# Kernel tuning notes

Measured on AMD Instinct MI355X. Metric: run time of the kernel, lower is better.

## Reference

```python
import jax, jax.numpy as jnp
import numpy as np

BETA = 0.25


def setup_inputs() -> dict:
    key = jax.random.key(0)
    k1, k2 = jax.random.split(key)
    z = jax.random.normal(k1, (16, 1024, 256), dtype=jnp.float32)
    embedding = jax.random.normal(k2, (8192, 256), dtype=jnp.float32)
    return {"z": z, "embedding": embedding}


def reference(z, embedding):
    e_dim = embedding.shape[-1]
    z_flat = jnp.reshape(z, (-1, e_dim))  # [N, e_dim]
    # d[i,k] = ||z_i||^2 + ||e_k||^2 - 2 z_i . e_k  -> [N, n_e]
    d = (jnp.sum(z_flat ** 2, axis=1, keepdims=True)
         + jnp.sum(embedding ** 2, axis=1)
         - 2.0 * jnp.einsum('nd,kd->nk', z_flat, embedding))
    min_encoding_indices = jnp.argmin(d, axis=1)  # [N]
    z_q = embedding[min_encoding_indices]
    z_q = jnp.reshape(z_q, z.shape)
    loss = (jnp.mean((jax.lax.stop_gradient(z_q) - z) ** 2)
            + BETA * jnp.mean((z_q - jax.lax.stop_gradient(z)) ** 2))
    z_q = z + jax.lax.stop_gradient(z_q - z)  # straight-through estimator
    return (z_q, loss, min_encoding_indices)
```

## Files before the change

kernel.cpp:

```cpp
#include <hip/hip_runtime.h>
#include <stdint.h>

#define N_ROWS   16384
#define DIM      256
#define N_CODES  8192
#define ZQ_ELEMS 4194304

typedef _Float16 f16x8 __attribute__((ext_vector_type(8)));
typedef _Float16 f16x4 __attribute__((ext_vector_type(4)));
typedef float    f32x16 __attribute__((ext_vector_type(16)));
typedef unsigned long long u64;

#define WS_ET  0
#define WS_PK  (8650752)

static __device__ __forceinline__ u64 packkey(float d, int c) {
    unsigned int u = __float_as_uint(d);
    u ^= ((unsigned int)((int)u >> 31)) | 0x80000000u;
    return ((u64)u << 32) | (unsigned int)c;
}

__global__ void vq_prep(const float* __restrict__ emb, _Float16* __restrict__ et,
                        float* __restrict__ loss_ptr) {
    __shared__ _Float16 sh[2][32][272];
    const int t = threadIdx.x, w = t >> 6, l = t & 63;
    if (blockIdx.x == 0 && t == 0) *loss_ptr = 0.0f;
    const int code0 = blockIdx.x * 32;
    #pragma unroll
    for (int j = 0; j < 8; ++j) {
        const int cl = w * 8 + j;
        float4 v = *(const float4*)(emb + (size_t)(code0 + cl) * DIM + l * 4);
        float xs[4] = {v.x, v.y, v.z, v.w};
        f16x4 hh, lo;
        float s = 0.0f;
        #pragma unroll
        for (int i = 0; i < 4; ++i) {
            _Float16 h = (_Float16)xs[i];
            hh[i] = h;
            lo[i] = (_Float16)(xs[i] - (float)h);
            s += xs[i] * xs[i];
        }
        *(f16x4*)&sh[0][cl][l * 4] = hh;
        *(f16x4*)&sh[1][cl][l * 4] = lo;
        #pragma unroll
        for (int off = 32; off > 0; off >>= 1) s += __shfl_down(s, off, 64);
        if (l == 0) {
            _Float16 nh = (_Float16)s;
            _Float16 nl = (_Float16)(s - (float)nh);
            f16x8 aug;
            #pragma unroll
            for (int i = 0; i < 8; ++i) aug[i] = (_Float16)0;
            aug[0] = nh; aug[1] = nl;
            *(f16x8*)(et + ((size_t)524288 + code0 + cl) * 8) = aug;
        }
    }
    __syncthreads();
    #pragma unroll
    for (int pp = 0; pp < 8; ++pp) {
        const int gi = pp * 256 + t;
        const int p = gi >> 10, ks = (gi >> 6) & 15, cl = (gi >> 1) & 31, h = gi & 1;
        f16x8 frag = *(const f16x8*)&sh[p][cl][ks * 16 + h * 8];
        const size_t unit = (size_t)p * 262144 + (size_t)ks * 16384
                          + (size_t)(code0 + cl) * 2 + h;
        *(f16x8*)(et + unit * 8) = frag;
    }
}

__global__ __launch_bounds__(512, 4)
void vq_main(const float* __restrict__ z, const _Float16* __restrict__ et,
             u64* __restrict__ pkeys) {
    extern __shared__ char smem[];
    u64* run = (u64*)(smem + 66560);

    const int tid = threadIdx.x;
    const int w = tid >> 6, L = tid & 63, lo5 = L & 31, hi1 = L >> 5;
    const int rb = blockIdx.x >> 1, sp = blockIdx.x & 1;
    const int row0 = rb * 64, codeS = sp * 4096;

    const float* zr = z + (size_t)row0 * DIM;
    #pragma unroll
    for (int jj = 0; jj < 8; ++jj) {
        const int idx = jj * 512 + tid;
        const int r = idx >> 6, q = idx & 63;
        float4 v = *(const float4*)(zr + (size_t)r * DIM + q * 4);
        float xs[4] = {v.x, v.y, v.z, v.w};
        f16x4 hh, lo;
        #pragma unroll
        for (int i = 0; i < 4; ++i) {
            const float m2 = -2.0f * xs[i];
            _Float16 h = (_Float16)m2;
            hh[i] = h;
            lo[i] = (_Float16)(m2 - (float)h);
        }
        char* base = smem + r * 1040 + q * 8;
        *(f16x4*)(base) = hh;
        *(f16x4*)(base + 512) = lo;
    }
    run[tid] = ~0ULL;

    f16x8 bz;
    #pragma unroll
    for (int i = 0; i < 8; ++i) bz[i] = (_Float16)0;
    if (hi1 == 0) { bz[0] = (_Float16)1; bz[1] = (_Float16)1; }

    f32x16 zacc;
    #pragma unroll
    for (int e = 0; e < 16; ++e) zacc[e] = 0.0f;

    const f16x8* eb  = (const f16x8*)et;
    const f16x8* ebL = eb + 262144;
    const int laneU = lo5 * 2 + hi1;
    const char* zb = smem + (lo5 * 1040 + hi1 * 16);

    f16x8 paug[2];
    {
        const int c0 = codeS + w * 64;
        paug[0] = eb[(size_t)524288 + c0 + lo5];
        paug[1] = eb[(size_t)524288 + c0 + 32 + lo5];
    }
    __syncthreads();

    for (int ci = 0; ci < 8; ++ci) {
        const int c0 = codeS + ci * 512 + w * 64;
        f32x16 acc[2][2];

        __builtin_amdgcn_s_setprio(1);
        #pragma unroll
        for (int mt = 0; mt < 2; ++mt)
            #pragma unroll
            for (int nt = 0; nt < 2; ++nt)
                acc[mt][nt] = __builtin_amdgcn_mfma_f32_32x32x16_f16(paug[mt], bz, zacc, 0, 0, 0);
        __builtin_amdgcn_s_setprio(0);

        if (ci < 7) {
            const int c1 = codeS + (ci + 1) * 512 + w * 64;
            paug[0] = eb[(size_t)524288 + c1 + lo5];
            paug[1] = eb[(size_t)524288 + c1 + 32 + lo5];
        }

        const size_t cu = (size_t)c0 * 2 + laneU;
        #pragma unroll 4
        for (int ksg = 0; ksg < 16; ++ksg) {
            const size_t ub = (size_t)ksg * 16384 + cu;
            f16x8 ah[2], al[2];
            ah[0] = eb[ub];       ah[1] = eb[ub + 64];
            al[0] = ebL[ub];      al[1] = ebL[ub + 64];
            f16x8 bh[2], bl[2];
            #pragma unroll
            for (int nt = 0; nt < 2; ++nt) {
                bh[nt] = *(const f16x8*)(zb + (ksg * 32 + nt * 33280));
                bl[nt] = *(const f16x8*)(zb + (ksg * 32 + nt * 33280 + 512));
            }
            __builtin_amdgcn_s_setprio(1);
            #pragma unroll
            for (int mt = 0; mt < 2; ++mt)
                #pragma unroll
                for (int nt = 0; nt < 2; ++nt) {
                    acc[mt][nt] = __builtin_amdgcn_mfma_f32_32x32x16_f16(ah[mt], bh[nt], acc[mt][nt], 0, 0, 0);
                    acc[mt][nt] = __builtin_amdgcn_mfma_f32_32x32x16_f16(ah[mt], bl[nt], acc[mt][nt], 0, 0, 0);
                    acc[mt][nt] = __builtin_amdgcn_mfma_f32_32x32x16_f16(al[mt], bh[nt], acc[mt][nt], 0, 0, 0);
                }
            __builtin_amdgcn_s_setprio(0);
        }

        #pragma unroll
        for (int nt = 0; nt < 2; ++nt) {
            float mm[16];
            #pragma unroll
            for (int r = 0; r < 16; ++r)
                mm[r] = fminf(acc[0][nt][r], acc[1][nt][r]);
            #pragma unroll
            for (int s2 = 8; s2 > 0; s2 >>= 1)
                #pragma unroll
                for (int r = 0; r < 8; ++r)
                    if (r < s2) mm[r] = fminf(mm[r], mm[r + s2]);
            const float m = mm[0];
            int rel = 64;
            #pragma unroll
            for (int mt = 0; mt < 2; ++mt)
                #pragma unroll
                for (int r = 0; r < 16; ++r) {
                    const int rc = mt * 32 + (r & 3) + 8 * (r >> 2);
                    const int cand = (acc[mt][nt][r] == m) ? rc : 64;
                    rel = cand < rel ? cand : rel;
                }
            u64 best = packkey(m, c0 + 4 * hi1 + rel);
            const u64 o = __shfl_xor(best, 32, 64);
            if (o < best) best = o;
            if (hi1 == 0) {
                u64* p = &run[w * 64 + nt * 32 + lo5];
                if (best < *p) *p = best;
            }
        }
    }

    __syncthreads();
    if (tid < 64) {
        u64 k = run[tid];
        #pragma unroll
        for (int w2 = 1; w2 < 8; ++w2) { u64 o = run[w2 * 64 + tid]; if (o < k) k = o; }
        pkeys[(size_t)sp * N_ROWS + row0 + tid] = k;
    }
}

__global__ __launch_bounds__(512)
void vq_final(const float* __restrict__ z, const float* __restrict__ emb,
              const u64* __restrict__ pkeys,
              float* __restrict__ zq_out, float* __restrict__ loss_out,
              float* __restrict__ idx_out) {
    __shared__ int best[64];
    const int t = threadIdx.x;
    const int row0 = blockIdx.x * 64;
    if (t < 64) {
        u64 k = pkeys[row0 + t];
        u64 o = pkeys[(size_t)N_ROWS + row0 + t];
        if (o < k) k = o;
        const int code = (int)(k & 0xFFFFFFFFu);
        best[t] = code;
        idx_out[row0 + t] = (float)code;
    }
    __syncthreads();
    const int wave = t >> 6, lane = t & 63;
    float lsum = 0.0f;
    #pragma unroll
    for (int rr = 0; rr < 8; ++rr) {
        const int rl = wave * 8 + rr;
        const int rg = row0 + rl;
        const int code = best[rl];
        float4 ev = *(const float4*)(emb + (size_t)code * DIM + lane * 4);
        float4 zv = *(const float4*)(z   + (size_t)rg   * DIM + lane * 4);
        float dx = ev.x - zv.x, dy = ev.y - zv.y;
        float dz = ev.z - zv.z, dw = ev.w - zv.w;
        lsum += dx * dx + dy * dy + dz * dz + dw * dw;
        *(float4*)(zq_out + (size_t)rg * DIM + lane * 4) = ev;
    }
    #pragma unroll
    for (int off = 32; off > 0; off >>= 1) lsum += __shfl_down(lsum, off, 64);
    if (lane == 0) atomicAdd(loss_out, lsum * (1.25f / (float)ZQ_ELEMS));
}

extern "C" void kernel_launch(void* const* d_in, const int* in_sizes, int n_in,
                              void* d_out, int out_size, void* d_ws, size_t ws_size,
                              hipStream_t stream) {
    const float* z   = (const float*)d_in[0];
    const float* emb = (const float*)d_in[1];
    float* out  = (float*)d_out;
    float* zq   = out;
    float* loss = out + ZQ_ELEMS;
    float* idx  = out + ZQ_ELEMS + 1;

    char* ws = (char*)d_ws;
    _Float16* et = (_Float16*)(ws + WS_ET);
    u64*   pk    = (u64*)(ws + WS_PK);

    static bool attr_set = false;
    if (!attr_set) {
        hipFuncSetAttribute((const void*)vq_main,
                            hipFuncAttributeMaxDynamicSharedMemorySize, 70656);
        attr_set = true;
    }

    vq_prep<<<256, 256, 0, stream>>>(emb, et, loss);
    vq_main<<<512, 512, 70656, stream>>>(z, et, pk);
    vq_final<<<N_ROWS / 64, 512, 0, stream>>>(z, emb, pk, zq, loss, idx);
}
```

Before: 294.7 us.

## Split codebook four ways and fuse final gather via last-block atomic reduction

```diff
diff --git a/kernel.cpp b/kernel.cpp
--- a/kernel.cpp
+++ b/kernel.cpp
@@ -12,7 +12,8 @@
 typedef unsigned long long u64;
 
 #define WS_ET  0
-#define WS_PK  (8650752)
+#define WS_PK  (8519680)
+#define WS_CNT (8650752)
 
 static __device__ __forceinline__ u64 packkey(float d, int c) {
     unsigned int u = __float_as_uint(d);
@@ -21,11 +22,15 @@
 }
 
 __global__ void vq_prep(const float* __restrict__ emb, _Float16* __restrict__ et,
+                        u64* __restrict__ pkeys, unsigned int* __restrict__ cnt,
                         float* __restrict__ loss_ptr) {
     __shared__ _Float16 sh[2][32][272];
     const int t = threadIdx.x, w = t >> 6, l = t & 63;
     if (blockIdx.x == 0 && t == 0) *loss_ptr = 0.0f;
+    if (t == 0) cnt[blockIdx.x] = 0;
+    if (t < 64) pkeys[blockIdx.x * 64 + t] = ~0ULL;
     const int code0 = blockIdx.x * 32;
+    const int sp0 = code0 >> 11, cw0 = code0 & 2047;
     #pragma unroll
     for (int j = 0; j < 8; ++j) {
         const int cl = w * 8 + j;
@@ -60,22 +65,26 @@
         const int gi = pp * 256 + t;
         const int p = gi >> 10, ks = (gi >> 6) & 15, cl = (gi >> 1) & 31, h = gi & 1;
         f16x8 frag = *(const f16x8*)&sh[p][cl][ks * 16 + h * 8];
-        const size_t unit = (size_t)p * 262144 + (size_t)ks * 16384
-                          + (size_t)(code0 + cl) * 2 + h;
+        const size_t unit = (size_t)p * 262144 + (size_t)sp0 * 65536
+                          + (size_t)ks * 4096 + (size_t)(cw0 + cl) * 2 + h;
         *(f16x8*)(et + unit * 8) = frag;
     }
 }
 
 __global__ __launch_bounds__(512, 4)
-void vq_main(const float* __restrict__ z, const _Float16* __restrict__ et,
-             u64* __restrict__ pkeys) {
+void vq_main(const float* __restrict__ z, const float* __restrict__ emb,
+             const _Float16* __restrict__ et, u64* __restrict__ pkeys,
+             unsigned int* __restrict__ cnt,
+             float* __restrict__ zq_out, float* __restrict__ loss_out,
+             float* __restrict__ idx_out) {
     extern __shared__ char smem[];
     u64* run = (u64*)(smem + 66560);
+    int* bestsh = (int*)(smem + 66560);
 
     const int tid = threadIdx.x;
     const int w = tid >> 6, L = tid & 63, lo5 = L & 31, hi1 = L >> 5;
-    const int rb = blockIdx.x >> 1, sp = blockIdx.x & 1;
-    const int row0 = rb * 64, codeS = sp * 4096;
+    const int rb = blockIdx.x >> 2, sp = blockIdx.x & 3;
+    const int row0 = rb * 64, codeS = sp * 2048;
 
     const float* zr = z + (size_t)row0 * DIM;
     #pragma unroll
@@ -110,6 +119,7 @@
     const f16x8* eb  = (const f16x8*)et;
     const f16x8* ebL = eb + 262144;
     const int laneU = lo5 * 2 + hi1;
+    const size_t spB = (size_t)sp * 65536;
     const char* zb = smem + (lo5 * 1040 + hi1 * 16);
 
     f16x8 paug[2];
@@ -120,8 +130,9 @@
     }
     __syncthreads();
 
-    for (int ci = 0; ci < 8; ++ci) {
+    for (int ci = 0; ci < 4; ++ci) {
         const int c0 = codeS + ci * 512 + w * 64;
+        const size_t cu = spB + (size_t)(ci * 512 + w * 64) * 2 + laneU;
         f32x16 acc[2][2];
 
         __builtin_amdgcn_s_setprio(1);
@@ -132,16 +143,15 @@
                 acc[mt][nt] = __builtin_amdgcn_mfma_f32_32x32x16_f16(paug[mt], bz, zacc, 0, 0, 0);
         __builtin_amdgcn_s_setprio(0);
 
-        if (ci < 7) {
+        if (ci < 3) {
             const int c1 = codeS + (ci + 1) * 512 + w * 64;
             paug[0] = eb[(size_t)524288 + c1 + lo5];
             paug[1] = eb[(size_t)524288 + c1 + 32 + lo5];
         }
 
-        const size_t cu = (size_t)c0 * 2 + laneU;
         #pragma unroll 4
         for (int ksg = 0; ksg < 16; ++ksg) {
-            const size_t ub = (size_t)ksg * 16384 + cu;
+            const size_t ub = cu + (size_t)ksg * 4096;
             f16x8 ah[2], al[2];
             ah[0] = eb[ub];       ah[1] = eb[ub + 64];
             al[0] = ebL[ub];      al[1] = ebL[ub + 64];
@@ -199,44 +209,39 @@
         u64 k = run[tid];
         #pragma unroll
         for (int w2 = 1; w2 < 8; ++w2) { u64 o = run[w2 * 64 + tid]; if (o < k) k = o; }
-        pkeys[(size_t)sp * N_ROWS + row0 + tid] = k;
-    }
-}
-
-__global__ __launch_bounds__(512)
-void vq_final(const float* __restrict__ z, const float* __restrict__ emb,
-              const u64* __restrict__ pkeys,
-              float* __restrict__ zq_out, float* __restrict__ loss_out,
-              float* __restrict__ idx_out) {
-    __shared__ int best[64];
-    const int t = threadIdx.x;
-    const int row0 = blockIdx.x * 64;
-    if (t < 64) {
-        u64 k = pkeys[row0 + t];
-        u64 o = pkeys[(size_t)N_ROWS + row0 + t];
-        if (o < k) k = o;
-        const int code = (int)(k & 0xFFFFFFFFu);
-        best[t] = code;
-        idx_out[row0 + t] = (float)code;
-    }
-    __syncthreads();
-    const int wave = t >> 6, lane = t & 63;
-    float lsum = 0.0f;
-    #pragma unroll
-    for (int rr = 0; rr < 8; ++rr) {
-        const int rl = wave * 8 + rr;
-        const int rg = row0 + rl;
-        const int code = best[rl];
-        float4 ev = *(const float4*)(emb + (size_t)code * DIM + lane * 4);
-        float4 zv = *(const float4*)(z   + (size_t)rg   * DIM + lane * 4);
-        float dx = ev.x - zv.x, dy = ev.y - zv.y;
-        float dz = ev.z - zv.z, dw = ev.w - zv.w;
-        lsum += dx * dx + dy * dy + dz * dz + dw * dw;
-        *(float4*)(zq_out + (size_t)rg * DIM + lane * 4) = ev;
-    }
-    #pragma unroll
-    for (int off = 32; off > 0; off >>= 1) lsum += __shfl_down(lsum, off, 64);
-    if (lane == 0) atomicAdd(loss_out, lsum * (1.25f / (float)ZQ_ELEMS));
+        atomicMin(&pkeys[row0 + tid], k);
+    }
+    __threadfence();
+    __syncthreads();
+
+    __shared__ int lastflag;
+    if (tid == 0) lastflag = (atomicAdd(&cnt[rb], 1u) == 3u) ? 1 : 0;
+    __syncthreads();
+    if (lastflag) {
+        if (tid < 64) {
+            const u64 k = atomicMin(&pkeys[row0 + tid], ~0ULL);
+            const int code = (int)(k & 0xFFFFFFFFu);
+            bestsh[tid] = code;
+            idx_out[row0 + tid] = (float)code;
+        }
+        __syncthreads();
+        float lsum = 0.0f;
+        #pragma unroll
+        for (int rr = 0; rr < 8; ++rr) {
+            const int rl = w * 8 + rr;
+            const int rg = row0 + rl;
+            const int code = bestsh[rl];
+            float4 ev = *(const float4*)(emb + (size_t)code * DIM + L * 4);
+            float4 zv = *(const float4*)(z   + (size_t)rg   * DIM + L * 4);
+            float dx = ev.x - zv.x, dy = ev.y - zv.y;
+            float dz = ev.z - zv.z, dw = ev.w - zv.w;
+            lsum += dx * dx + dy * dy + dz * dz + dw * dw;
+            *(float4*)(zq_out + (size_t)rg * DIM + L * 4) = ev;
+        }
+        #pragma unroll
+        for (int off = 32; off > 0; off >>= 1) lsum += __shfl_down(lsum, off, 64);
+        if (L == 0) atomicAdd(loss_out, lsum * (1.25f / (float)ZQ_ELEMS));
+    }
 }
 
 extern "C" void kernel_launch(void* const* d_in, const int* in_sizes, int n_in,
@@ -252,6 +257,7 @@
     char* ws = (char*)d_ws;
     _Float16* et = (_Float16*)(ws + WS_ET);
     u64*   pk    = (u64*)(ws + WS_PK);
+    unsigned int* cn = (unsigned int*)(ws + WS_CNT);
 
     static bool attr_set = false;
     if (!attr_set) {
@@ -260,7 +266,6 @@
         attr_set = true;
     }
 
-    vq_prep<<<256, 256, 0, stream>>>(emb, et, loss);
-    vq_main<<<512, 512, 70656, stream>>>(z, et, pk);
-    vq_final<<<N_ROWS / 64, 512, 0, stream>>>(z, emb, pk, zq, loss, idx);
-}
+    vq_prep<<<256, 256, 0, stream>>>(emb, et, pk, cn, loss);
+    vq_main<<<1024, 512, 70656, stream>>>(z, emb, et, pk, cn, zq, loss, idx);
+}
```

New measurement: 441.6 us. 1.5x slower.
